# Performance work log

Hardware: AMD Instinct MI355X
Metric: run time of the kernel (lower is better)

## Reference

```python
import jax, jax.numpy as jnp
import numpy as np
from jax import lax

B, T, F0 = 16, 1024, 128
L_CNN, L_RNN, D = 3, 3, 512
NF = F0 // 2  # 64, freq dim after stride-2 conv
EPS = 1e-5


def conv2d(x, w, b, stride, pad):
    # x: [B,C,H,W], w: [O,I,kh,kw]
    y = lax.conv_general_dilated(x, w, (stride, stride), [(pad, pad), (pad, pad)],
                                 dimension_numbers=('NCHW', 'OIHW', 'NCHW'))
    return y + b[None, :, None, None]


def ln_last(x, g, b):
    m = x.mean(-1, keepdims=True)
    v = ((x - m) ** 2).mean(-1, keepdims=True)
    return (x - m) * lax.rsqrt(v + EPS) * g + b


def ln_feats(x, g, b):
    # LayerNorm over freq axis (axis 2) of [B,C,F,T] (== transpose(2,3); LN; transpose back)
    m = x.mean(2, keepdims=True)
    v = ((x - m) ** 2).mean(2, keepdims=True)
    return (x - m) * lax.rsqrt(v + EPS) * g[None, None, :, None] + b[None, None, :, None]


def sru_dir(u, x_res, v, b, reverse):
    # u: [T,B,3,D] (candidate, f-pre, r-pre); x_res: [T,B,D] highway input; v,b: [2,D]
    u0 = u[:, :, 0]
    fp = u[:, :, 1] + b[0]
    rp = u[:, :, 2] + b[1]

    def step(c, inp):
        u0t, fpt, rpt, xrt = inp
        f = jax.nn.sigmoid(fpt + v[0] * c)
        r = jax.nn.sigmoid(rpt + v[1] * c)
        c = f * c + (1.0 - f) * u0t
        h = r * jnp.tanh(c) + (1.0 - r) * xrt
        return c, h

    c0 = jnp.zeros(u0.shape[1:], u.dtype)
    _, h = lax.scan(step, c0, (u0, fp, rp, x_res), reverse=reverse)
    return h  # [T,B,D]


def _forward(x, cnn_w, cnn_b, res_w1, res_b1, res_w2, res_b2,
             res_ln1_g, res_ln1_b, res_ln2_g, res_ln2_b,
             proj_w, sru_w, sru_v, sru_b, sru_ln_g, sru_ln_b,
             cls_ln_g, cls_ln_b, cls_w1, cls_b1, cls_w2, cls_b2):
    # stem conv: [B,1,128,1024] -> [B,32,64,512]
    x = conv2d(x, cnn_w, cnn_b, 2, 1)
    # residual CNN blocks (dropout = identity in eval)
    for i in range(L_CNN):
        res = x
        h = jax.nn.relu(ln_feats(x, res_ln1_g[i], res_ln1_b[i]))
        h = conv2d(h, res_w1[i], res_b1[i], 1, 1)
        h = jax.nn.relu(ln_feats(h, res_ln2_g[i], res_ln2_b[i]))
        h = conv2d(h, res_w2[i], res_b2[i], 1, 1)
        x = h + res
    # flatten channels x freq, time-major: [T', B, 32*NF]
    b_, c_, f_, t_ = x.shape
    x = x.reshape(b_, c_ * f_, t_).transpose(2, 0, 1)
    # proj_input_to_hidden_first: 2048 -> 2*D
    x = jnp.einsum('tbi,ih->tbh', x, proj_w)
    # bidirectional SRU layers
    for l in range(L_RNN):
        xl = ln_last(x, sru_ln_g[l], sru_ln_b[l])
        # u: [T,B,dir,gate,D]
        u = jnp.einsum('tbi,idkh->tbdkh', xl, sru_w[l])
        h_f = sru_dir(u[:, :, 0], x[..., :D], sru_v[l, 0], sru_b[l, 0], False)
        h_b = sru_dir(u[:, :, 1], x[..., D:], sru_v[l, 1], sru_b[l, 1], True)
        x = jnp.concatenate([h_f, h_b], axis=-1)
    # classifier: [B, T', 2D] -> [B, T', n_vocab+1]
    x = x.transpose(1, 0, 2)
    x = ln_last(x, cls_ln_g, cls_ln_b)
    x = jax.nn.relu(jnp.einsum('bth,hd->btd', x, cls_w1) + cls_b1)
    x = jnp.einsum('btd,dv->btv', x, cls_w2) + cls_b2
    return x


def setup_inputs() -> dict:
    key = jax.random.key(0)
    ks = iter(jax.random.split(key, 40))

    def rn(shape, s=0.05):
        return jax.random.normal(next(ks), shape, jnp.float32) * s

    return dict(
        x=jax.random.normal(next(ks), (B, 1, F0, T), jnp.float32),
        cnn_w=rn((32, 1, 3, 3)), cnn_b=jnp.zeros(32, jnp.float32),
        res_w1=rn((L_CNN, 32, 32, 3, 3)), res_b1=jnp.zeros((L_CNN, 32), jnp.float32),
        res_w2=rn((L_CNN, 32, 32, 3, 3)), res_b2=jnp.zeros((L_CNN, 32), jnp.float32),
        res_ln1_g=jnp.ones((L_CNN, NF), jnp.float32), res_ln1_b=jnp.zeros((L_CNN, NF), jnp.float32),
        res_ln2_g=jnp.ones((L_CNN, NF), jnp.float32), res_ln2_b=jnp.zeros((L_CNN, NF), jnp.float32),
        proj_w=rn((NF * 32, 2 * D), 0.02),
        sru_w=rn((L_RNN, 2 * D, 2, 3, D), 0.02),
        sru_v=rn((L_RNN, 2, 2, D), 0.1),
        sru_b=jnp.zeros((L_RNN, 2, 2, D), jnp.float32),
        sru_ln_g=jnp.ones((L_RNN, 2 * D), jnp.float32), sru_ln_b=jnp.zeros((L_RNN, 2 * D), jnp.float32),
        cls_ln_g=jnp.ones(2 * D, jnp.float32), cls_ln_b=jnp.zeros(2 * D, jnp.float32),
        cls_w1=rn((2 * D, D), 0.02), cls_b1=jnp.zeros(D, jnp.float32),
        cls_w2=rn((D, 29), 0.02), cls_b2=jnp.zeros(29, jnp.float32),
    )


def reference(x, cnn_w, cnn_b, res_w1, res_b1, res_w2, res_b2,
              res_ln1_g, res_ln1_b, res_ln2_g, res_ln2_b,
              proj_w, sru_w, sru_v, sru_b, sru_ln_g, sru_ln_b,
              cls_ln_g, cls_ln_b, cls_w1, cls_b1, cls_w2, cls_b2):
    return _forward(x, cnn_w, cnn_b, res_w1, res_b1, res_w2, res_b2,
                    res_ln1_g, res_ln1_b, res_ln2_g, res_ln2_b,
                    proj_w, sru_w, sru_v, sru_b, sru_ln_g, sru_ln_b,
                    cls_ln_g, cls_ln_b, cls_w1, cls_b1, cls_w2, cls_b2)
```

## Files before the change

kernel.cpp:

```cpp
#include <hip/hip_runtime.h>

typedef unsigned short u16;
typedef unsigned int u32;
typedef __attribute__((ext_vector_type(8))) short short8;
typedef __attribute__((ext_vector_type(4))) float floatx4;

__device__ __forceinline__ float bf2f(u16 u) {
    union { unsigned int i; float f; } v; v.i = ((unsigned int)u) << 16; return v.f;
}
__device__ __forceinline__ u16 f2bf(float f) {
    union { float f; unsigned int i; } v; v.f = f;
    unsigned int i = v.i + 0x7fffu + ((v.i >> 16) & 1u);
    return (u16)(i >> 16);
}

#define GLL(g, l) __builtin_amdgcn_global_load_lds( \
    (const __attribute__((address_space(1))) void*)(g), \
    (__attribute__((address_space(3))) void*)(l), 16, 0, 0)

#define WAITVM(n) asm volatile("s_waitcnt vmcnt(" #n ")" ::: "memory")

#define HA_BSTRIDE 1085568

__global__ __launch_bounds__(256) void sniff_k(const u16* __restrict__ x, int* __restrict__ flag) {
    __shared__ int red[4];
    int cnt = 0;
    for (int i = 0; i < 16; ++i) {
        u16 v = x[(threadIdx.x * 16 + i) * 2];
        int e = (v >> 7) & 0xFF;
        if (e >= 110 && e <= 135) cnt++;
    }
    #pragma unroll
    for (int off = 32; off; off >>= 1) cnt += __shfl_down(cnt, off);
    if ((threadIdx.x & 63) == 0) red[threadIdx.x >> 6] = cnt;
    __syncthreads();
    if (threadIdx.x == 0) {
        int tot = red[0] + red[1] + red[2] + red[3];
        *flag = (tot < 2048) ? 1 : 0;
    }
}

__device__ __forceinline__ float ldin(const void* p, size_t i, int isf32) {
    return isf32 ? ((const float*)p)[i] : bf2f(((const u16*)p)[i]);
}

struct CvtArgs {
    const void* src[19];
    int len[19];
    int off[19];
};
__global__ __launch_bounds__(256) void cvtall_k(CvtArgs a, float* __restrict__ dst,
                                                const int* __restrict__ flag) {
    int isf32 = *flag;
    int seg = blockIdx.y;
    int n = a.len[seg];
    const void* s = a.src[seg];
    float* d = dst + a.off[seg];
    for (int i = blockIdx.x * 256 + threadIdx.x; i < n; i += gridDim.x * 256)
        d[i] = ldin(s, i, isf32);
}

__global__ __launch_bounds__(256) void wtr_k(const void* __restrict__ W, int ldw, size_t wofs,
                                             u16* __restrict__ Wt, int ldt,
                                             const int* __restrict__ flag) {
    int isf32 = *flag;
    __shared__ u16 t[64][65];
    int k0 = blockIdx.x * 64, n0 = blockIdx.y * 64;
    int tid = threadIdx.x;
    #pragma unroll
    for (int i = 0; i < 16; ++i) {
        int kk = i * 4 + (tid >> 6), nn = tid & 63;
        t[kk][nn] = f2bf(ldin(W, wofs + (size_t)(k0 + kk) * ldw + n0 + nn, isf32));
    }
    __syncthreads();
    #pragma unroll
    for (int i = 0; i < 16; ++i) {
        int nn = i * 4 + (tid >> 6), kk = tid & 63;
        Wt[(size_t)(n0 + nn) * ldt + k0 + kk] = t[kk][nn];
    }
}

__global__ __launch_bounds__(256) void zero_k(float4* __restrict__ p, int n4) {
    float4 z = {0.f, 0.f, 0.f, 0.f};
    for (int i = blockIdx.x * 256 + threadIdx.x; i < n4; i += gridDim.x * 256) p[i] = z;
}
__global__ __launch_bounds__(256) void fill_k(float* __restrict__ p, int n) {
    int i = blockIdx.x * 256 + threadIdx.x;
    if (i < n) p[i] = 1.0e6f;
}

__global__ __launch_bounds__(256) void conv1_k(const void* __restrict__ x, const float* __restrict__ w,
                                               const float* __restrict__ bias, float* __restrict__ out,
                                               const int* __restrict__ flag) {
    int isf32 = *flag;
    int idx = blockIdx.x * 256 + threadIdx.x;
    int t  = idx & 511;
    int f  = (idx >> 9) & 63;
    int cg = (idx >> 15) & 7;
    int b  = idx >> 18;
    size_t xb = (size_t)b * 128 * 1024;

    float wr[4][9];
    #pragma unroll
    for (int i = 0; i < 4; ++i)
        #pragma unroll
        for (int k = 0; k < 9; ++k) wr[i][k] = w[(cg * 4 + i) * 9 + k];

    float acc[4];
    #pragma unroll
    for (int i = 0; i < 4; ++i) acc[i] = bias[cg * 4 + i];

    #pragma unroll
    for (int df = 0; df < 3; ++df) {
        int fi = 2 * f + df - 1;
        if (fi < 0 || fi >= 128) continue;
        size_t rowb = xb + (size_t)fi * 1024;
        float xv[3];
        #pragma unroll
        for (int dt = 0; dt < 3; ++dt) {
            int ti = 2 * t + dt - 1;
            float v = 0.f;
            if (ti >= 0 && ti < 1024) v = ldin(x, rowb + ti, isf32);
            xv[dt] = v;
        }
        #pragma unroll
        for (int i = 0; i < 4; ++i)
            #pragma unroll
            for (int dt = 0; dt < 3; ++dt)
                acc[i] = fmaf(wr[i][df * 3 + dt], xv[dt], acc[i]);
    }
    size_t obase = (((size_t)b * 32 + cg * 4) * 64 + f) * 512 + t;
    #pragma unroll
    for (int i = 0; i < 4; ++i) out[obase + (size_t)i * 64 * 512] = acc[i];
}

__global__ __launch_bounds__(256) void stats_k(const void* __restrict__ X, int isbf,
                                               float* __restrict__ sm, float* __restrict__ sr) {
    int idx = blockIdx.x * 256 + threadIdx.x;
    int t  = idx & 511;
    int bc = idx >> 9;
    size_t base = (size_t)bc * 64 * 512 + t;
    float s = 0.f, s2 = 0.f;
    #pragma unroll 8
    for (int f = 0; f < 64; ++f) {
        float v = isbf ? bf2f(((const u16*)X)[base + f * 512]) : ((const float*)X)[base + f * 512];
        s += v; s2 += v * v;
    }
    float m  = s * (1.f / 64.f);
    float var = fmaxf(s2 * (1.f / 64.f) - m * m, 0.f);
    sm[idx] = m;
    sr[idx] = rsqrtf(var + 1e-5f);
}

__global__ __launch_bounds__(256) void apply_k(const void* __restrict__ in, int isbf,
                                               const float* __restrict__ sm, const float* __restrict__ sr,
                                               const float* __restrict__ g, const float* __restrict__ be,
                                               u16* __restrict__ Ha) {
    int f = blockIdx.x;
    int b = blockIdx.y;
    float gg = g[f], bb_ = be[f];
    for (int it = 0; it < 2; ++it) {
        int t = it * 256 + threadIdx.x;
        u32 pk[16];
        #pragma unroll
        for (int cp = 0; cp < 16; ++cp) {
            u32 w = 0;
            #pragma unroll
            for (int half = 0; half < 2; ++half) {
                int ci = cp * 2 + half;
                size_t xi = (((size_t)b * 32 + ci) * 64 + f) * 512 + t;
                float xv = isbf ? bf2f(((const u16*)in)[xi]) : ((const float*)in)[xi];
                int si = (b * 32 + ci) * 512 + t;
                float hv = fmaxf((xv - sm[si]) * sr[si] * gg + bb_, 0.f);
                w |= ((u32)f2bf(hv)) << (half * 16);
            }
            pk[cp] = w;
        }
        u32* orow = (u32*)(Ha + (size_t)b * HA_BSTRIDE + ((size_t)(f + 1) * 514 + (t + 1)) * 32);
        #pragma unroll
        for (int q = 0; q < 16; ++q) orow[q] = pk[q];
    }
}

__global__ __launch_bounds__(256) void convm_k(const u16* __restrict__ Ha, void* __restrict__ out,
                                               const float* __restrict__ w, const float* __restrict__ bias,
                                               const float* __restrict__ res) {
    __shared__ u16 act[34 * 18 * 32];
    int F0 = blockIdx.x * 32;
    int t0 = blockIdx.y * 16;
    int b  = blockIdx.z;
    const u16* Hb = Ha + (size_t)b * HA_BSTRIDE;
    int tid  = threadIdx.x;
    int lane = tid & 63;
    int wv   = tid >> 6;
    int quad = lane >> 4;
    int r    = lane & 15;

    #pragma unroll
    for (int it = 0; it < 10; ++it) {
        int u = it * 256 + tid;
        if (u < 2448) {
            int fp  = u / 72;
            int rem = u - fp * 72;
            int tp  = rem >> 2;
            int q   = rem & 3;
            GLL(Hb + ((size_t)(F0 + fp) * 514 + (t0 + tp)) * 32 + q * 8, act + u * 8);
        }
    }

    short8 bfrag[3][3][2];
    #pragma unroll
    for (int df = 0; df < 3; ++df)
        #pragma unroll
        for (int dt = 0; dt < 3; ++dt)
            #pragma unroll
            for (int ct = 0; ct < 2; ++ct) {
                short8 v;
                #pragma unroll
                for (int j = 0; j < 8; ++j) {
                    int co = ct * 16 + r, ci = quad * 8 + j;
                    v[j] = (short)f2bf(w[(co * 32 + ci) * 9 + df * 3 + dt]);
                }
                bfrag[df][dt][ct] = v;
            }
    __syncthreads();

    #pragma unroll
    for (int sub = 0; sub < 2; ++sub) {
        floatx4 acc[4][2];
        #pragma unroll
        for (int i = 0; i < 4; ++i)
            #pragma unroll
            for (int j = 0; j < 2; ++j)
                #pragma unroll
                for (int k = 0; k < 4; ++k) acc[i][j][k] = 0.f;

        int fb = wv * 8 + sub * 4;
        #pragma unroll
        for (int fh = 0; fh < 6; ++fh) {
            short8 af[3];
            #pragma unroll
            for (int dt = 0; dt < 3; ++dt)
                af[dt] = *(const short8*)&act[(((fb + fh) * 18) + (r + dt)) * 32 + quad * 8];
            #pragma unroll
            for (int df = 0; df < 3; ++df) {
                int rel = fh - df;
                if (rel < 0 || rel >= 4) continue;
                #pragma unroll
                for (int dt = 0; dt < 3; ++dt)
                    #pragma unroll
                    for (int ct = 0; ct < 2; ++ct)
                        acc[rel][ct] = __builtin_amdgcn_mfma_f32_16x16x32_bf16(
                            af[dt], bfrag[df][dt][ct], acc[rel][ct], 0, 0, 0);
            }
        }

        int tt = t0 + quad * 4;
        #pragma unroll
        for (int rel = 0; rel < 4; ++rel)
            #pragma unroll
            for (int ct = 0; ct < 2; ++ct) {
                int f  = F0 + fb + rel;
                int co = ct * 16 + r;
                size_t base = (((size_t)b * 32 + co) * 64 + f) * 512 + tt;
                float bs = bias[co];
                if (res) {
                    float4 rv = *(const float4*)(res + base);
                    float4 o;
                    o.x = acc[rel][ct][0] + bs + rv.x;
                    o.y = acc[rel][ct][1] + bs + rv.y;
                    o.z = acc[rel][ct][2] + bs + rv.z;
                    o.w = acc[rel][ct][3] + bs + rv.w;
                    *(float4*)((float*)out + base) = o;
                } else {
                    ushort4 o;
                    o.x = f2bf(acc[rel][ct][0] + bs);
                    o.y = f2bf(acc[rel][ct][1] + bs);
                    o.z = f2bf(acc[rel][ct][2] + bs);
                    o.w = f2bf(acc[rel][ct][3] + bs);
                    *(ushort4*)((u16*)out + base) = o;
                }
            }
    }
}

__global__ __launch_bounds__(256) void transpose_k(const float* __restrict__ X, u16* __restrict__ A) {
    __shared__ float tile[64][65];
    int t0 = blockIdx.x * 64;
    int c  = blockIdx.y;
    int b  = blockIdx.z;
    const float* p = X + (((size_t)b * 32 + c) * 64) * 512 + t0;
    #pragma unroll
    for (int i = 0; i < 16; ++i) {
        int f = i * 4 + (threadIdx.x >> 6);
        int t = threadIdx.x & 63;
        tile[f][t] = p[(size_t)f * 512 + t];
    }
    __syncthreads();
    #pragma unroll
    for (int i = 0; i < 16; ++i) {
        int t = i * 4 + (threadIdx.x >> 6);
        int f = threadIdx.x & 63;
        A[((size_t)(t0 + t) * 16 + b) * 2048 + c * 64 + f] = f2bf(tile[f][t]);
    }
}

__global__ __launch_bounds__(256) void lnlast_k(const float* __restrict__ X, u16* __restrict__ Y,
                                                const float* __restrict__ g, const float* __restrict__ bt,
                                                int width) {
    int row = blockIdx.x;
    const float* p = X + (size_t)row * width;
    float s = 0.f, s2 = 0.f;
    for (int i = threadIdx.x; i < width; i += 256) { float v = p[i]; s += v; s2 += v * v; }
    #pragma unroll
    for (int off = 32; off; off >>= 1) { s += __shfl_down(s, off); s2 += __shfl_down(s2, off); }
    __shared__ float red[4][2];
    int wv = threadIdx.x >> 6;
    if ((threadIdx.x & 63) == 0) { red[wv][0] = s; red[wv][1] = s2; }
    __syncthreads();
    if (threadIdx.x == 0) {
        float a = 0.f, b2 = 0.f;
        for (int i = 0; i < 4; ++i) { a += red[i][0]; b2 += red[i][1]; }
        float m = a / width;
        float var = fmaxf(b2 / width - m * m, 0.f);
        red[0][0] = m; red[0][1] = rsqrtf(var + 1e-5f);
    }
    __syncthreads();
    float m = red[0][0], rs = red[0][1];
    u16* q = Y + (size_t)row * width;
    for (int i = threadIdx.x; i < width; i += 256)
        q[i] = f2bf((p[i] - m) * rs * g[i] + bt[i]);
}

__global__ __launch_bounds__(256) void gemm_bt(const u16* __restrict__ A, const u16* __restrict__ A2,
                                               int lda, const u16* __restrict__ Bt, int ldb,
                                               void* __restrict__ C, void* __restrict__ C2,
                                               int ldc, int nsplit,
                                               const float* __restrict__ bias, int relu, int K,
                                               int obf) {
    __shared__ u16 As[128 * 32];
    __shared__ u16 Bs[128 * 32];
    int tid  = threadIdx.x;
    int bm   = blockIdx.x * 128;
    int bn   = blockIdx.y * 128;
    const u16* Ab = A;
    void* Cb = C;
    int cn = bn;
    if (bn >= nsplit) { Ab = A2; Cb = C2; cn = bn - nsplit; }

    int lane = tid & 63;
    int wv   = tid >> 6;
    int quad = lane >> 4;
    int r    = lane & 15;
    int wm   = (wv >> 1) * 64;
    int wn   = (wv & 1) * 64;

    floatx4 acc[4][4];
    #pragma unroll
    for (int i = 0; i < 4; ++i)
        #pragma unroll
        for (int j = 0; j < 4; ++j)
            #pragma unroll
            for (int k = 0; k < 4; ++k) acc[i][j][k] = 0.f;

    int row0 = tid >> 2;
    int ks0  = ((tid & 3) ^ ((tid >> 3) & 3)) * 8;
    const u16* Abase  = Ab + (size_t)(bm + row0) * lda + ks0;
    const u16* Abase2 = Ab + (size_t)(bm + 64 + row0) * lda + ks0;
    const u16* Bbase  = Bt + (size_t)(bn + row0) * ldb + ks0;
    const u16* Bbase2 = Bt + (size_t)(bn + 64 + row0) * ldb + ks0;
    u16* AsD  = As + tid * 8;
    u16* AsD2 = As + 2048 + tid * 8;
    u16* BsD  = Bs + tid * 8;
    u16* BsD2 = Bs + 2048 + tid * 8;

    for (int k0 = 0; k0 < K; k0 += 32) {
        GLL(Abase + k0, AsD);
        GLL(Abase2 + k0, AsD2);
        GLL(Bbase + k0, BsD);
        GLL(Bbase2 + k0, BsD2);
        __syncthreads();
        int col = (quad ^ ((r >> 1) & 3)) * 8;
        short8 af[4], bf[4];
        #pragma unroll
        for (int mi = 0; mi < 4; ++mi) af[mi] = *(const short8*)&As[(wm + mi * 16 + r) * 32 + col];
        #pragma unroll
        for (int ni = 0; ni < 4; ++ni) bf[ni] = *(const short8*)&Bs[(wn + ni * 16 + r) * 32 + col];
        #pragma unroll
        for (int mi = 0; mi < 4; ++mi)
            #pragma unroll
            for (int ni = 0; ni < 4; ++ni)
                acc[mi][ni] = __builtin_amdgcn_mfma_f32_16x16x32_bf16(af[mi], bf[ni], acc[mi][ni], 0, 0, 0);
        __syncthreads();
    }

    #pragma unroll
    for (int mi = 0; mi < 4; ++mi)
        #pragma unroll
        for (int ni = 0; ni < 4; ++ni) {
            int col = cn + wn + ni * 16 + r;
            float bs = bias ? bias[col] : 0.f;
            #pragma unroll
            for (int reg = 0; reg < 4; ++reg) {
                int row = bm + wm + mi * 16 + quad * 4 + reg;
                float v = acc[mi][ni][reg] + bs;
                if (relu) v = fmaxf(v, 0.f);
                if (obf) ((u16*)Cb)[(size_t)row * ldc + col] = f2bf(v);
                else     ((float*)Cb)[(size_t)row * ldc + col] = v;
            }
        }
}

#define TC 256
__global__ __launch_bounds__(64) void scan_k(const u16* __restrict__ Uf, const u16* __restrict__ Ub,
                                             const float* __restrict__ Xp, float* __restrict__ Xn,
                                             float* __restrict__ cstate, const float* __restrict__ vv,
                                             const float* __restrict__ bb, int t0f, int t0b, int init) {
    __shared__ __align__(16) char lds[4][10240];
    int tid = threadIdx.x;
    int d   = blockIdx.x >> 7;
    int idx = blockIdx.x & 127;
    int b   = idx >> 3;
    int h0  = (idx & 7) * 64;
    int h   = h0 + tid;
    int gid = d * 8192 + idx * 64 + tid;

    float v0 = vv[(d * 2 + 0) * 512 + h];
    float v1 = vv[(d * 2 + 1) * 512 + h];
    float b0 = bb[(d * 2 + 0) * 512 + h];
    float b1 = bb[(d * 2 + 1) * 512 + h];
    const u16* U = d ? Ub : Uf;
    int t0 = d ? t0b : t0f;
    float* ob = Xn + (size_t)b * 1024 + d * 512 + h;
    float cc = init ? 0.f : cstate[gid];
    int tstp = d ? -16384 : 16384;

    const char* gp[10];
    int dlt[10];
    #pragma unroll
    for (int it = 0; it < 10; ++it) {
        int u = it * 64 + tid;
        int s = u / 40;
        int j = u - s * 40;
        int sl0 = d ? (TC - 1 - s) : s;
        if (j < 24) {
            int k = j >> 3, jj = j & 7;
            gp[it] = (const char*)(U + ((size_t)(sl0 * 16 + b) * 1536 + k * 512 + h0 + jj * 8));
            dlt[it] = d ? -786432 : 786432;
        } else {
            gp[it] = (const char*)(Xp + ((size_t)(t0 + sl0) * 16384 + (size_t)b * 1024 + d * 512 + h0 + (j - 24) * 4));
            dlt[it] = d ? -1048576 : 1048576;
        }
    }
    char* lbase = (char*)&lds[0][0] + tid * 16;
    auto stage = [&](int bw) {
        char* lb = lbase + bw * 10240;
        #pragma unroll
        for (int it = 0; it < 10; ++it) {
            GLL(gp[it], lb + it * 1024);
            gp[it] += dlt[it];
        }
    };

    asm volatile("s_waitcnt vmcnt(0)" ::: "memory");
    __builtin_amdgcn_sched_barrier(0);
    stage(0);
    stage(1);
    stage(2);
    __builtin_amdgcn_sched_barrier(0);

    #pragma unroll 1
    for (int tk = 0; tk < 16; ++tk) {
        switch (tk) {
            case 0:  WAITVM(20); break;
            case 1:  WAITVM(36); break;
            case 14: WAITVM(42); break;
            case 15: WAITVM(32); break;
            default: WAITVM(52); break;
        }
        __builtin_amdgcn_sched_barrier(0);
        const char* Bb = (const char*)&lds[0][0] + (size_t)(tk & 3) * 10240;
        float* op = ob + (size_t)(t0 + (d ? (TC - 1 - tk * 16) : tk * 16)) * 16384;
        #pragma unroll
        for (int s = 0; s < 16; ++s) {
            const char* sb = Bb + s * 640;
            float u0 = bf2f(*(const u16*)(sb + tid * 2));
            float fp = bf2f(*(const u16*)(sb + 128 + tid * 2)) + b0;
            float rp = bf2f(*(const u16*)(sb + 256 + tid * 2)) + b1;
            float xr = *(const float*)(sb + 384 + tid * 4);
            float f = 1.f / (1.f + __expf(-(fp + v0 * cc)));
            float r = 1.f / (1.f + __expf(-(rp + v1 * cc)));
            cc = f * cc + (1.f - f) * u0;
            float th = 1.f - 2.f / (__expf(2.f * cc) + 1.f);
            *op = r * th + (1.f - r) * xr;
            op += tstp;
        }
        __builtin_amdgcn_sched_barrier(0);
        if (tk < 13) stage((tk + 3) & 3);
        __builtin_amdgcn_sched_barrier(0);
    }
    cstate[gid] = cc;
}

__global__ __launch_bounds__(256) void cls2_k(const float* __restrict__ FC1, const float* __restrict__ W2,
                                              const float* __restrict__ b2, void* __restrict__ out,
                                              const int* __restrict__ flag) {
    int isf32 = *flag;
    int row = blockIdx.x * 4 + (threadIdx.x >> 6);
    int v   = threadIdx.x & 63;
    if (v >= 29) return;
    const float* p = FC1 + (size_t)row * 512;
    float acc = 0.f;
    for (int k = 0; k < 512; ++k) acc = fmaf(p[k], W2[k * 29 + v], acc);
    acc += b2[v];
    int t = row >> 4, b = row & 15;
    size_t oi = ((size_t)b * 512 + t) * 29 + v;
    if (isf32) ((float*)out)[oi] = acc;
    else       ((u16*)out)[oi]   = f2bf(acc);
}

extern "C" void kernel_launch(void* const* d_in, const int* in_sizes, int n_in,
                              void* d_out, int out_size, void* d_ws, size_t ws_size,
                              hipStream_t stream) {
    const void* x      = d_in[0];
    const void* proj_w = d_in[11];
    const void* sru_w  = d_in[12];
    const void* cls_w1 = d_in[19];

    float* ws = (float*)d_ws;
    const size_t O_X    = 0;
    const size_t O_C    = 16777216;
    const size_t O_HA   = 25165824;
    const size_t O_SM   = 33850368;
    const size_t O_SR   = 34112512;
    const size_t O_CST  = 34374656;
    const size_t O_PARK = 34391040;
    const size_t O_FLAG = 34483488;
    const size_t TOTAL  = 34483504;
    if (ws_size < TOTAL * sizeof(float)) {
        fill_k<<<(out_size + 255) / 256, 256, 0, stream>>>((float*)d_out, out_size);
        return;
    }

    float* X   = ws + O_X;
    u16*   C   = (u16*)(ws + O_C);
    u16*   HA  = (u16*)(ws + O_HA);
    float* SM  = ws + O_SM;
    float* SR  = ws + O_SR;
    float* CST = ws + O_CST;
    float* PK  = ws + O_PARK;
    int*   FLG = (int*)(ws + O_FLAG);

    u16*   Abf = (u16*)(ws + O_C);
    u16*   BtP = (u16*)(ws + 0);
    float* XP0 = ws + 25165824;
    u16*   XL  = (u16*)(ws + 0);
    float* XP1 = ws + 4194304;
    u16*   Uf  = (u16*)(ws + 12582912);
    u16*   Ub  = (u16*)(ws + 15728640);
    u16*   BtS = (u16*)(ws + 18874368);
    u16*   BtC = (u16*)(ws + O_SM);
    float* FC1 = ws + 12582912;

    float* p_cnn_w = PK + 0;      float* p_cnn_b = PK + 288;
    float* p_rw1   = PK + 320;    float* p_rb1   = PK + 27968;
    float* p_rw2   = PK + 28064;  float* p_rb2   = PK + 55712;
    float* p_l1g   = PK + 55808;  float* p_l1b   = PK + 56000;
    float* p_l2g   = PK + 56192;  float* p_l2b   = PK + 56384;
    float* p_sv    = PK + 56576;  float* p_sb    = PK + 62720;
    float* p_slng  = PK + 68864;  float* p_slnb  = PK + 71936;
    float* p_clng  = PK + 75008;  float* p_clnb  = PK + 76032;
    float* p_cb1   = PK + 77056;  float* p_cw2   = PK + 77568;
    float* p_cb2   = PK + 92416;

    sniff_k<<<1, 256, 0, stream>>>((const u16*)x, FLG);

    CvtArgs ca;
    const int srcidx[19] = {1,2,3,4,5,6,7,8,9,10,13,14,15,16,17,18,20,21,22};
    const int lens[19]   = {288,32,27648,96,27648,96,192,192,192,192,6144,6144,3072,3072,1024,1024,512,14848,29};
    const int offs[19]   = {0,288,320,27968,28064,55712,55808,56000,56192,56384,56576,62720,68864,71936,75008,76032,77056,77568,92416};
    for (int i = 0; i < 19; ++i) { ca.src[i] = d_in[srcidx[i]]; ca.len[i] = lens[i]; ca.off[i] = offs[i]; }
    cvtall_k<<<dim3(108, 19), 256, 0, stream>>>(ca, PK, FLG);

    zero_k<<<2048, 256, 0, stream>>>((float4*)HA, 2171136);
    conv1_k<<<16384, 256, 0, stream>>>(x, p_cnn_w, p_cnn_b, X, FLG);

    for (int i = 0; i < 3; ++i) {
        stats_k<<<1024, 256, 0, stream>>>(X, 0, SM, SR);
        apply_k<<<dim3(64, 16), 256, 0, stream>>>(X, 0, SM, SR, p_l1g + i * 64, p_l1b + i * 64, HA);
        convm_k<<<dim3(2, 32, 16), 256, 0, stream>>>(HA, C, p_rw1 + i * 9216, p_rb1 + i * 32, nullptr);
        stats_k<<<1024, 256, 0, stream>>>(C, 1, SM, SR);
        apply_k<<<dim3(64, 16), 256, 0, stream>>>(C, 1, SM, SR, p_l2g + i * 64, p_l2b + i * 64, HA);
        convm_k<<<dim3(2, 32, 16), 256, 0, stream>>>(HA, X, p_rw2 + i * 9216, p_rb2 + i * 32, X);
    }

    transpose_k<<<dim3(8, 32, 16), 256, 0, stream>>>(X, Abf);
    wtr_k<<<dim3(32, 16), 256, 0, stream>>>(proj_w, 1024, 0, BtP, 2048, FLG);
    gemm_bt<<<dim3(64, 8), 256, 0, stream>>>(Abf, Abf, 2048, BtP, 2048, XP0, XP0, 1024,
                                             1 << 30, nullptr, 0, 2048, 0);

    for (int l = 0; l < 3; ++l)
        wtr_k<<<dim3(16, 48), 256, 0, stream>>>(sru_w, 3072, (size_t)l * 3145728,
                                                BtS + (size_t)l * 3145728, 1024, FLG);
    wtr_k<<<dim3(16, 8), 256, 0, stream>>>(cls_w1, 512, 0, BtC, 1024, FLG);

    float* cur = XP0;
    float* nxt = XP1;
    for (int l = 0; l < 3; ++l) {
        lnlast_k<<<8192, 256, 0, stream>>>(cur, XL, p_slng + l * 1024, p_slnb + l * 1024, 1024);
        const u16* Btl = BtS + (size_t)l * 3145728;
        for (int j = 0; j < 2; ++j) {
            int t0f = j * TC;
            int t0b = (1 - j) * TC;
            gemm_bt<<<dim3(32, 24), 256, 0, stream>>>(XL + (size_t)t0f * 16 * 1024,
                                                      XL + (size_t)t0b * 16 * 1024, 1024,
                                                      Btl, 1024, Uf, Ub, 1536, 1536,
                                                      nullptr, 0, 1024, 1);
            scan_k<<<256, 64, 0, stream>>>(Uf, Ub, cur, nxt, CST,
                                           p_sv + l * 2048, p_sb + l * 2048, t0f, t0b, j == 0);
        }
        float* tmp = cur; cur = nxt; nxt = tmp;
    }

    lnlast_k<<<8192, 256, 0, stream>>>(cur, XL, p_clng, p_clnb, 1024);
    gemm_bt<<<dim3(64, 4), 256, 0, stream>>>(XL, XL, 1024, BtC, 1024, FC1, FC1, 512,
                                             1 << 30, p_cb1, 1, 1024, 0);
    cls2_k<<<2048, 256, 0, stream>>>(FC1, p_cw2, p_cb2, d_out, FLG);
}
```

Before: 1.462 ms.

## Double-buffer conv tiles across time loop and split classifier reduction across lanes

The residual conv kernel now processes four consecutive 16-step time tiles per block, with a block covering 16 frequency rows instead of 32. The next tile's activations are loaded into LDS asynchronously while the current tile computes, and the bf16 weight fragments are reused across all four tiles. The intent is to hide global-load latency and amortise per-block weight conversion. The final classifier kernel splits the K=512 dot product over four lane groups with a shuffle and LDS reduction, which raises parallelism and coalescing. In exchange, the conv path depends on hand-tuned vmcnt wait counts and extra barriers, and both kernels get a different grid shape.

Result: faster. 1.427 ms (-2.3%).

```diff
diff --git a/kernel.cpp b/kernel.cpp
--- a/kernel.cpp
+++ b/kernel.cpp
@@ -19,6 +19,7 @@
     (__attribute__((address_space(3))) void*)(l), 16, 0, 0)
 
 #define WAITVM(n) asm volatile("s_waitcnt vmcnt(" #n ")" ::: "memory")
+#define SBAR() __builtin_amdgcn_sched_barrier(0)
 
 #define HA_BSTRIDE 1085568
 
@@ -182,31 +183,41 @@
     }
 }
 
+#define CVL 4
 __global__ __launch_bounds__(256) void convm_k(const u16* __restrict__ Ha, void* __restrict__ out,
                                                const float* __restrict__ w, const float* __restrict__ bias,
                                                const float* __restrict__ res) {
-    __shared__ u16 act[34 * 18 * 32];
-    int F0 = blockIdx.x * 32;
-    int t0 = blockIdx.y * 16;
-    int b  = blockIdx.z;
+    __shared__ __align__(16) u16 act[2][1536 * 8];
+    int F0    = blockIdx.x * 16;
+    int tbase = blockIdx.y * 64;
+    int b     = blockIdx.z;
     const u16* Hb = Ha + (size_t)b * HA_BSTRIDE;
     int tid  = threadIdx.x;
     int lane = tid & 63;
     int wv   = tid >> 6;
     int quad = lane >> 4;
     int r    = lane & 15;
-
-    #pragma unroll
-    for (int it = 0; it < 10; ++it) {
+    int hasres = (res != nullptr);
+
+    int ufp[6], utp[6], uq[6];
+    #pragma unroll
+    for (int it = 0; it < 6; ++it) {
         int u = it * 256 + tid;
-        if (u < 2448) {
-            int fp  = u / 72;
-            int rem = u - fp * 72;
-            int tp  = rem >> 2;
-            int q   = rem & 3;
-            GLL(Hb + ((size_t)(F0 + fp) * 514 + (t0 + tp)) * 32 + q * 8, act + u * 8);
-        }
-    }
+        int u2 = (u < 1296) ? u : (u - 1296);
+        int fp = u2 / 72;
+        int rem = u2 - fp * 72;
+        ufp[it] = fp; utp[it] = rem >> 2; uq[it] = rem & 3;
+    }
+
+    auto stage = [&](int tile, int bw) {
+        int t00 = tbase + tile * 16;
+        #pragma unroll
+        for (int it = 0; it < 6; ++it) {
+            int u = it * 256 + tid;
+            GLL(Hb + ((size_t)(F0 + ufp[it]) * 514 + (t00 + utp[it])) * 32 + uq[it] * 8,
+                &act[bw][u * 8]);
+        }
+    };
 
     short8 bfrag[3][3][2];
     #pragma unroll
@@ -223,25 +234,39 @@
                 }
                 bfrag[df][dt][ct] = v;
             }
-    __syncthreads();
-
-    #pragma unroll
-    for (int sub = 0; sub < 2; ++sub) {
+
+    WAITVM(0);
+    SBAR();
+    stage(0, 0);
+    SBAR();
+
+    int fb = wv * 4;
+    #pragma unroll 1
+    for (int i = 0; i < CVL; ++i) {
+        if (i < CVL - 1) stage(i + 1, (i + 1) & 1);
+        SBAR();
+        if (i == 0)            { WAITVM(6); }
+        else if (i < CVL - 1)  { if (hasres) WAITVM(22); else WAITVM(14); }
+        else                   { if (hasres) WAITVM(16); else WAITVM(8); }
+        SBAR();
+        __builtin_amdgcn_s_barrier();
+        SBAR();
+
+        const u16* ab = act[i & 1];
         floatx4 acc[4][2];
         #pragma unroll
-        for (int i = 0; i < 4; ++i)
+        for (int ii = 0; ii < 4; ++ii)
             #pragma unroll
             for (int j = 0; j < 2; ++j)
                 #pragma unroll
-                for (int k = 0; k < 4; ++k) acc[i][j][k] = 0.f;
-
-        int fb = wv * 8 + sub * 4;
+                for (int k = 0; k < 4; ++k) acc[ii][j][k] = 0.f;
+
         #pragma unroll
         for (int fh = 0; fh < 6; ++fh) {
             short8 af[3];
             #pragma unroll
             for (int dt = 0; dt < 3; ++dt)
-                af[dt] = *(const short8*)&act[(((fb + fh) * 18) + (r + dt)) * 32 + quad * 8];
+                af[dt] = *(const short8*)&ab[((fb + fh) * 18 + (r + dt)) * 32 + quad * 8];
             #pragma unroll
             for (int df = 0; df < 3; ++df) {
                 int rel = fh - df;
@@ -255,6 +280,7 @@
             }
         }
 
+        int t0 = tbase + i * 16;
         int tt = t0 + quad * 4;
         #pragma unroll
         for (int rel = 0; rel < 4; ++rel)
@@ -264,7 +290,7 @@
                 int co = ct * 16 + r;
                 size_t base = (((size_t)b * 32 + co) * 64 + f) * 512 + tt;
                 float bs = bias[co];
-                if (res) {
+                if (hasres) {
                     float4 rv = *(const float4*)(res + base);
                     float4 o;
                     o.x = acc[rel][ct][0] + bs + rv.x;
@@ -281,6 +307,9 @@
                     *(ushort4*)((u16*)out + base) = o;
                 }
             }
+        SBAR();
+        __builtin_amdgcn_s_barrier();
+        SBAR();
     }
 }
 
@@ -463,11 +492,11 @@
     };
 
     asm volatile("s_waitcnt vmcnt(0)" ::: "memory");
-    __builtin_amdgcn_sched_barrier(0);
+    SBAR();
     stage(0);
     stage(1);
     stage(2);
-    __builtin_amdgcn_sched_barrier(0);
+    SBAR();
 
     #pragma unroll 1
     for (int tk = 0; tk < 16; ++tk) {
@@ -478,7 +507,7 @@
             case 15: WAITVM(32); break;
             default: WAITVM(52); break;
         }
-        __builtin_amdgcn_sched_barrier(0);
+        SBAR();
         const char* Bb = (const char*)&lds[0][0] + (size_t)(tk & 3) * 10240;
         float* op = ob + (size_t)(t0 + (d ? (TC - 1 - tk * 16) : tk * 16)) * 16384;
         #pragma unroll
@@ -495,9 +524,9 @@
             *op = r * th + (1.f - r) * xr;
             op += tstp;
         }
-        __builtin_amdgcn_sched_barrier(0);
+        SBAR();
         if (tk < 13) stage((tk + 3) & 3);
-        __builtin_amdgcn_sched_barrier(0);
+        SBAR();
     }
     cstate[gid] = cc;
 }
@@ -506,17 +535,30 @@
                                               const float* __restrict__ b2, void* __restrict__ out,
                                               const int* __restrict__ flag) {
     int isf32 = *flag;
-    int row = blockIdx.x * 4 + (threadIdx.x >> 6);
-    int v   = threadIdx.x & 63;
-    if (v >= 29) return;
-    const float* p = FC1 + (size_t)row * 512;
+    int tid = threadIdx.x;
+    int rh = tid >> 7;
+    int ks = (tid >> 5) & 3;
+    int v  = tid & 31;
+    int row = blockIdx.x * 2 + rh;
+    const float* p = FC1 + (size_t)row * 512 + ks * 128;
+    const float* wp = W2 + (size_t)ks * 128 * 29;
     float acc = 0.f;
-    for (int k = 0; k < 512; ++k) acc = fmaf(p[k], W2[k * 29 + v], acc);
-    acc += b2[v];
-    int t = row >> 4, b = row & 15;
-    size_t oi = ((size_t)b * 512 + t) * 29 + v;
-    if (isf32) ((float*)out)[oi] = acc;
-    else       ((u16*)out)[oi]   = f2bf(acc);
+    #pragma unroll 4
+    for (int k = 0; k < 128; ++k) {
+        float wv = (v < 29) ? wp[k * 29 + v] : 0.f;
+        acc = fmaf(p[k], wv, acc);
+    }
+    acc += __shfl_xor(acc, 32);
+    __shared__ float red[2][2][32];
+    if ((tid & 63) < 32) red[rh][(tid >> 6) & 1][v] = acc;
+    __syncthreads();
+    if ((tid & 127) < 32 && v < 29) {
+        float s = red[rh][0][v] + red[rh][1][v] + b2[v];
+        int t = row >> 4, b = row & 15;
+        size_t oi = ((size_t)b * 512 + t) * 29 + v;
+        if (isf32) ((float*)out)[oi] = s;
+        else       ((u16*)out)[oi]   = f2bf(s);
+    }
 }
 
 extern "C" void kernel_launch(void* const* d_in, const int* in_sizes, int n_in,
@@ -588,10 +630,10 @@
     for (int i = 0; i < 3; ++i) {
         stats_k<<<1024, 256, 0, stream>>>(X, 0, SM, SR);
         apply_k<<<dim3(64, 16), 256, 0, stream>>>(X, 0, SM, SR, p_l1g + i * 64, p_l1b + i * 64, HA);
-        convm_k<<<dim3(2, 32, 16), 256, 0, stream>>>(HA, C, p_rw1 + i * 9216, p_rb1 + i * 32, nullptr);
+        convm_k<<<dim3(4, 8, 16), 256, 0, stream>>>(HA, C, p_rw1 + i * 9216, p_rb1 + i * 32, nullptr);
         stats_k<<<1024, 256, 0, stream>>>(C, 1, SM, SR);
         apply_k<<<dim3(64, 16), 256, 0, stream>>>(C, 1, SM, SR, p_l2g + i * 64, p_l2b + i * 64, HA);
-        convm_k<<<dim3(2, 32, 16), 256, 0, stream>>>(HA, X, p_rw2 + i * 9216, p_rb2 + i * 32, X);
+        convm_k<<<dim3(4, 8, 16), 256, 0, stream>>>(HA, X, p_rw2 + i * 9216, p_rb2 + i * 32, X);
     }
 
     transpose_k<<<dim3(8, 32, 16), 256, 0, stream>>>(X, Abf);
@@ -625,5 +667,5 @@
     lnlast_k<<<8192, 256, 0, stream>>>(cur, XL, p_clng, p_clnb, 1024);
     gemm_bt<<<dim3(64, 4), 256, 0, stream>>>(XL, XL, 1024, BtC, 1024, FC1, FC1, 512,
                                              1 << 30, p_cb1, 1, 1024, 0);
-    cls2_k<<<2048, 256, 0, stream>>>(FC1, p_cw2, p_cb2, d_out, FLG);
-}
+    cls2_k<<<4096, 256, 0, stream>>>(FC1, p_cw2, p_cb2, d_out, FLG);
+}
```
